# Optimization experiments

Hardware: AMD Instinct MI355X
Metric: run time of the kernel (lower is better)

Reference implementation:

```python
import jax, jax.numpy as jnp
import numpy as np

N = 100000  # number of nodes
SELF_LOOP_W = 2.0  # improved=True in PyG GCNConv


def gcn_conv(x, edge_index, W, b):
    # x: [N, Fin], edge_index: [2, E] (row=src, col=dst), W: [Fin, Fout], b: [Fout]
    src, dst = edge_index[0], edge_index[1]
    h = x @ W  # [N, Fout]
    # degree with improved self-loops (weight 2.0)
    ones = jnp.ones(src.shape, dtype=h.dtype)
    deg = jax.ops.segment_sum(ones, dst, num_segments=N) + SELF_LOOP_W
    dinv = jnp.where(deg > 0, jax.lax.rsqrt(deg), 0.0)
    norm = dinv[src] * dinv[dst]  # [E]
    agg = jax.ops.segment_sum(h[src] * norm[:, None], dst, num_segments=N)
    # self-loop contribution: weight 2.0, norm = dinv_i * 2 * dinv_i
    agg = agg + h * (SELF_LOOP_W * dinv * dinv)[:, None]
    return agg + b


def setup_inputs() -> dict:
    key = jax.random.key(0)
    ks = jax.random.split(key, 6)
    x = jax.random.normal(ks[0], (N, 64), dtype=jnp.float32)
    edge_index = jax.random.randint(ks[1], (2, 1600000), 0, N, dtype=jnp.int64)
    W1 = jax.random.normal(ks[2], (64, 64), dtype=jnp.float32) * 0.1
    b1 = jax.random.normal(ks[3], (64,), dtype=jnp.float32) * 0.1
    W2 = jax.random.normal(ks[4], (64, 32), dtype=jnp.float32) * 0.1
    b2 = jax.random.normal(ks[5], (32,), dtype=jnp.float32) * 0.1
    return {"x": x, "edge_index": edge_index, "W1": W1, "b1": b1, "W2": W2, "b2": b2}


def reference(x, edge_index, W1, b1, W2, b2):
    h1 = jax.nn.relu(gcn_conv(x, edge_index, W1, b1))
    feature_map = h1
    out = gcn_conv(h1, edge_index, W2, b2)
    return (out, feature_map)
```

## Files before the change

kernel.cpp:

```cpp
#include <hip/hip_runtime.h>

#define N_NODES 100000
#define E_EDGES 1600000

#define BSHIFT 7
#define BSIZE 128
#define NBUCK ((N_NODES + BSIZE - 1) / BSIZE)
#define STAGE_TPB 512
#define STAGE_EPT 8
#define STAGE_CHUNK (STAGE_TPB * STAGE_EPT)
#define NREP 2
#define BUCKET_CAP 4096

typedef __attribute__((ext_vector_type(8))) short short8;
typedef __attribute__((ext_vector_type(4))) float float4v;
typedef __attribute__((ext_vector_type(4))) int int4v;
typedef __attribute__((ext_vector_type(4))) unsigned uint4v;

__device__ inline unsigned short f2bf(float f) {
    union { float f; unsigned u; } t; t.f = f;
    unsigned r = (t.u + 0x7fffu + ((t.u >> 16) & 1u)) >> 16;
    return (unsigned short)r;
}
__device__ inline float bf2f(unsigned short h) {
    union { unsigned u; float f; } t; t.u = ((unsigned)h) << 16; return t.f;
}
__device__ inline unsigned pack_bf16x2(float a, float b) {
    return (unsigned)f2bf(a) | ((unsigned)f2bf(b) << 16);
}
__device__ inline float bf_lo(unsigned u) { union { unsigned u; float f; } t; t.u = u << 16; return t.f; }
__device__ inline float bf_hi(unsigned u) { union { unsigned u; float f; } t; t.u = u & 0xffff0000u; return t.f; }

__global__ void cursor_init_kernel(int* __restrict__ gcursor,
                                   unsigned* __restrict__ HS1, unsigned* __restrict__ HS2) {
    int b = blockIdx.x * blockDim.x + threadIdx.x;
    if (b < NBUCK) gcursor[b] = b * BUCKET_CAP;
    if (b < 32) HS1[(size_t)N_NODES * 32 + b] = 0u;
    if (b < 16) HS2[(size_t)N_NODES * 16 + b] = 0u;
}

__global__ void __launch_bounds__(STAGE_TPB) stage_kernel(
    const int* __restrict__ src, const int* __restrict__ dst,
    int* __restrict__ gcursor, unsigned* __restrict__ staged, int E) {
    __shared__ int hist[NREP][NBUCK];
    __shared__ int base[NREP][NBUCK];
    const int tid = threadIdx.x;
    const int rep = (tid >> 8) & (NREP - 1);
    const int e0 = blockIdx.x * STAGE_CHUNK;
    for (int i = tid; i < NREP * NBUCK; i += STAGE_TPB) ((int*)hist)[i] = 0;
    __syncthreads();
    int d[STAGE_EPT], s[STAGE_EPT];
#pragma unroll
    for (int k = 0; k < STAGE_EPT / 4; ++k) {
        int e = e0 + (k * STAGE_TPB + tid) * 4;
        if (e < E) {
            int4v sv = *(const int4v*)(src + e);
            int4v dv = *(const int4v*)(dst + e);
#pragma unroll
            for (int i = 0; i < 4; ++i) {
                s[4 * k + i] = sv[i];
                d[4 * k + i] = dv[i];
                atomicAdd(&hist[rep][dv[i] >> BSHIFT], 1);
            }
        } else {
#pragma unroll
            for (int i = 0; i < 4; ++i) d[4 * k + i] = -1;
        }
    }
    __syncthreads();
    for (int i = tid; i < NBUCK; i += STAGE_TPB) {
        int h0 = hist[0][i], h1 = hist[1][i];
        int t = h0 + h1;
        if (t > 0) {
            int g = atomicAdd(&gcursor[i], t);
            base[0][i] = g;
            base[1][i] = g + h0;
        }
    }
    __syncthreads();
#pragma unroll
    for (int k = 0; k < STAGE_EPT; ++k) {
        if (d[k] >= 0) {
            int b = d[k] >> BSHIFT;
            int pos = atomicAdd(&base[rep][b], 1);
            if (pos < (b + 1) * BUCKET_CAP)
                staged[pos] = (unsigned)s[k] | ((unsigned)(d[k] & (BSIZE - 1)) << 17);
        }
    }
}

__global__ void bscan_kernel(const int* __restrict__ gcursor, int* __restrict__ boff) {
    __shared__ int s[1024];
    const int tid = threadIdx.x;
    int v = 0;
    if (tid < NBUCK) {
        v = gcursor[tid] - tid * BUCKET_CAP;
        if (v > BUCKET_CAP) v = BUCKET_CAP;
        v = (v + 391) & ~3;
    }
    s[tid] = v;
    __syncthreads();
    for (int off = 1; off < 1024; off <<= 1) {
        int t = (tid >= off) ? s[tid - off] : 0;
        __syncthreads();
        s[tid] += t;
        __syncthreads();
    }
    if (tid < NBUCK) boff[tid] = s[tid] - v;
    if (tid == NBUCK - 1) boff[NBUCK] = s[tid];
}

__global__ void bucket_csr_kernel(const unsigned* __restrict__ staged,
                                  const int* __restrict__ gcursor,
                                  const int* __restrict__ boff,
                                  int2* __restrict__ nodeinfo, float* __restrict__ dinv,
                                  int* __restrict__ csrc, int n) {
    __shared__ int ldeg[BSIZE];
    __shared__ int laex[BSIZE];
    __shared__ int lscan[BSIZE];
    __shared__ int lcnt[BSIZE];
    __shared__ unsigned lrec[BUCKET_CAP];
    __shared__ int lsrc[BUCKET_CAP + 512];
    __shared__ int ltot;
    const int b = blockIdx.x;
    const int node0 = b * BSIZE;
    const int nn = min(BSIZE, n - node0);
    const int tid = threadIdx.x;
    if (tid < BSIZE) { ldeg[tid] = 0; lcnt[tid] = 0; }
    __syncthreads();
    const int ebase = boff[b];
    int ecnt = gcursor[b] - b * BUCKET_CAP;
    if (ecnt > BUCKET_CAP) ecnt = BUCKET_CAP;
    const int sbase = b * BUCKET_CAP;
    for (int i = tid; i < ecnt; i += 256) {
        unsigned r = staged[sbase + i];
        lrec[i] = r;
        atomicAdd(&ldeg[r >> 17], 1);
    }
    __syncthreads();
    int mydeg = (tid < BSIZE) ? ldeg[tid] : 0;
    int adeg = (mydeg + 3) & ~3;
    if (tid < BSIZE) lscan[tid] = adeg;
    __syncthreads();
    for (int off = 1; off < BSIZE; off <<= 1) {
        int v = 0;
        if (tid < BSIZE && tid >= off) v = lscan[tid - off];
        __syncthreads();
        if (tid < BSIZE) lscan[tid] += v;
        __syncthreads();
    }
    if (tid < BSIZE) {
        int aex = lscan[tid] - adeg;
        laex[tid] = aex;
        if (tid == BSIZE - 1) ltot = lscan[tid];
        if (tid < nn) {
            nodeinfo[node0 + tid] = make_int2(ebase + aex, mydeg);
            dinv[node0 + tid] = rsqrtf((float)mydeg + 2.0f);
            for (int k = mydeg; k < adeg; ++k) lsrc[aex + k] = N_NODES;
        }
    }
    __syncthreads();
    for (int i = tid; i < ecnt; i += 256) {
        unsigned r = lrec[i];
        int dl = (int)(r >> 17);
        int sv = (int)(r & 0x1FFFFu);
        int pos = laex[dl] + atomicAdd(&lcnt[dl], 1);
        if (pos < BUCKET_CAP + 512) lsrc[pos] = sv;
    }
    __syncthreads();
    const int tot = ltot;
    for (int i = tid; i < tot; i += 256)
        csrc[ebase + i] = lsrc[i];
}

template <int FOUT>
__global__ void __launch_bounds__(256) linear_mfma_kernel(
    const float* __restrict__ X, const float* __restrict__ W,
    const float* __restrict__ dinv, unsigned* __restrict__ HS, int n) {
    constexpr int NT = FOUT / 16;
    constexpr int ROWU = NT * 8;
    const int NTILES_M = n / 16;
    const int lane = threadIdx.x & 63;
    const int gwave = blockIdx.x * 4 + (threadIdx.x >> 6);
    const int nwaves = gridDim.x * 4;
    const int m = lane & 15;
    const int q = lane >> 4;

    short8 Bhi[2][NT], Blo[2][NT];
#pragma unroll
    for (int ks = 0; ks < 2; ++ks)
#pragma unroll
        for (int nt = 0; nt < NT; ++nt) {
            short8 bh, bl;
#pragma unroll
            for (int j = 0; j < 8; ++j) {
                int k = ks * 32 + q * 8 + j;
                float wv = W[k * FOUT + nt * 16 + m];
                unsigned short h = f2bf(wv);
                bh[j] = (short)h;
                bl[j] = (short)f2bf(wv - bf2f(h));
            }
            Bhi[ks][nt] = bh;
            Blo[ks][nt] = bl;
        }

    for (int tile = gwave; tile < NTILES_M; tile += nwaves) {
        const int row0 = tile * 16;
        float4v C[NT];
#pragma unroll
        for (int nt = 0; nt < NT; ++nt) C[nt] = (float4v){0.f, 0.f, 0.f, 0.f};
#pragma unroll
        for (int ks = 0; ks < 2; ++ks) {
            const float* xp = X + (size_t)(row0 + m) * 64 + ks * 32 + q * 8;
            float4v x0 = *(const float4v*)xp;
            float4v x1 = *(const float4v*)(xp + 4);
            short8 Ahi, Alo;
#pragma unroll
            for (int j = 0; j < 4; ++j) {
                unsigned short h0 = f2bf(x0[j]);
                Ahi[j] = (short)h0;
                Alo[j] = (short)f2bf(x0[j] - bf2f(h0));
                unsigned short h1 = f2bf(x1[j]);
                Ahi[4 + j] = (short)h1;
                Alo[4 + j] = (short)f2bf(x1[j] - bf2f(h1));
            }
#pragma unroll
            for (int nt = 0; nt < NT; ++nt) {
                C[nt] = __builtin_amdgcn_mfma_f32_16x16x32_bf16(Ahi, Bhi[ks][nt], C[nt], 0, 0, 0);
                C[nt] = __builtin_amdgcn_mfma_f32_16x16x32_bf16(Alo, Bhi[ks][nt], C[nt], 0, 0, 0);
                C[nt] = __builtin_amdgcn_mfma_f32_16x16x32_bf16(Ahi, Blo[ks][nt], C[nt], 0, 0, 0);
            }
        }
#pragma unroll
        for (int ch = 0; ch < NT / 2; ++ch) {
#pragma unroll
            for (int reg = 0; reg < 4; ++reg) {
                int r = row0 + q * 4 + reg;
                float di = dinv[r];
                unsigned u = pack_bf16x2(C[2 * ch][reg] * di, C[2 * ch + 1][reg] * di);
                HS[(size_t)r * ROWU + ch * 16 + m] = u;
            }
        }
    }
}

template <int ROWU, bool RELU>
__global__ void __launch_bounds__(256) gather_vec_kernel(
    const int2* __restrict__ nodeinfo, const int* __restrict__ csrc,
    const unsigned* __restrict__ HS, const float* __restrict__ dinv,
    const float* __restrict__ bias, float* __restrict__ OUT, int n) {
    constexpr int G = ROWU / 4;
    constexpr int NPB = 256 / G;
    constexpr int FOUT = ROWU * 2;
    const int node = blockIdx.x * NPB + (int)(threadIdx.x / G);
    const int t = threadIdx.x % G;
    if (node >= n) return;
    int2 ni = nodeinfo[node];
    const int start = ni.x;
    const int deg = ni.y;
    const int pend = start + ((deg + 3) & ~3);
    const unsigned* __restrict__ HSt = HS + 4 * t;
    const uint4v own = *(const uint4v*)(HS + (size_t)node * ROWU + 4 * t);
    float alo[4], ahi[4];
#pragma unroll
    for (int k = 0; k < 4; ++k) { alo[k] = 2.0f * bf_lo(own[k]); ahi[k] = 2.0f * bf_hi(own[k]); }
    int j = start;
    for (; j + 8 <= pend; j += 8) {
        int4v s0 = *(const int4v*)(csrc + j);
        int4v s1 = *(const int4v*)(csrc + j + 4);
        uint4v u0 = *(const uint4v*)(HSt + (size_t)s0[0] * ROWU);
        uint4v u1 = *(const uint4v*)(HSt + (size_t)s0[1] * ROWU);
        uint4v u2 = *(const uint4v*)(HSt + (size_t)s0[2] * ROWU);
        uint4v u3 = *(const uint4v*)(HSt + (size_t)s0[3] * ROWU);
        uint4v u4 = *(const uint4v*)(HSt + (size_t)s1[0] * ROWU);
        uint4v u5 = *(const uint4v*)(HSt + (size_t)s1[1] * ROWU);
        uint4v u6 = *(const uint4v*)(HSt + (size_t)s1[2] * ROWU);
        uint4v u7 = *(const uint4v*)(HSt + (size_t)s1[3] * ROWU);
#pragma unroll
        for (int k = 0; k < 4; ++k) {
            float l01 = bf_lo(u0[k]) + bf_lo(u1[k]);
            float l23 = bf_lo(u2[k]) + bf_lo(u3[k]);
            float l45 = bf_lo(u4[k]) + bf_lo(u5[k]);
            float l67 = bf_lo(u6[k]) + bf_lo(u7[k]);
            alo[k] += (l01 + l23) + (l45 + l67);
            float h01 = bf_hi(u0[k]) + bf_hi(u1[k]);
            float h23 = bf_hi(u2[k]) + bf_hi(u3[k]);
            float h45 = bf_hi(u4[k]) + bf_hi(u5[k]);
            float h67 = bf_hi(u6[k]) + bf_hi(u7[k]);
            ahi[k] += (h01 + h23) + (h45 + h67);
        }
    }
    if (j < pend) {
        int4v s0 = *(const int4v*)(csrc + j);
        uint4v u0 = *(const uint4v*)(HSt + (size_t)s0[0] * ROWU);
        uint4v u1 = *(const uint4v*)(HSt + (size_t)s0[1] * ROWU);
        uint4v u2 = *(const uint4v*)(HSt + (size_t)s0[2] * ROWU);
        uint4v u3 = *(const uint4v*)(HSt + (size_t)s0[3] * ROWU);
#pragma unroll
        for (int k = 0; k < 4; ++k) {
            alo[k] += (bf_lo(u0[k]) + bf_lo(u1[k])) + (bf_lo(u2[k]) + bf_lo(u3[k]));
            ahi[k] += (bf_hi(u0[k]) + bf_hi(u1[k])) + (bf_hi(u2[k]) + bf_hi(u3[k]));
        }
    }
    const float dd = dinv[node];
    const int ch = t >> 2;
    const int c0 = (4 * t) & 15;
    const float4v blv = *(const float4v*)(bias + 32 * ch + c0);
    const float4v bhv = *(const float4v*)(bias + 32 * ch + 16 + c0);
    float4v olo, ohi;
#pragma unroll
    for (int k = 0; k < 4; ++k) {
        float o0 = alo[k] * dd + blv[k];
        float o1 = ahi[k] * dd + bhv[k];
        if (RELU) { o0 = fmaxf(o0, 0.0f); o1 = fmaxf(o1, 0.0f); }
        olo[k] = o0;
        ohi[k] = o1;
    }
    float* op = OUT + (size_t)node * FOUT + 32 * ch + c0;
    *(float4v*)op = olo;
    *(float4v*)(op + 16) = ohi;
}

extern "C" void kernel_launch(void* const* d_in, const int* in_sizes, int n_in,
                              void* d_out, int out_size, void* d_ws, size_t ws_size,
                              hipStream_t stream) {
    const float* x  = (const float*)d_in[0];
    const int*   ei = (const int*)d_in[1];
    const float* W1 = (const float*)d_in[2];
    const float* b1 = (const float*)d_in[3];
    const float* W2 = (const float*)d_in[4];
    const float* b2 = (const float*)d_in[5];

    const int* srcp = ei;
    const int* dstp = ei + E_EDGES;

    float* out = (float*)d_out;
    float* fm  = (float*)d_out + N_NODES * 32;

    char* w = (char*)d_ws;
    int*      gcursor  = (int*)w;       w += sizeof(int) * NBUCK;
    int*      boff     = (int*)w;       w += sizeof(int) * (NBUCK + 1);
    int2*     nodeinfo = (int2*)w;      w += sizeof(int2) * N_NODES;
    float*    dinv     = (float*)w;     w += sizeof(float) * N_NODES;
    int*      csrc     = (int*)w;       w += sizeof(int) * (E_EDGES + NBUCK * 392);
    unsigned* staged   = (unsigned*)w;  w += sizeof(unsigned) * (size_t)NBUCK * BUCKET_CAP;
    unsigned* HS1      = (unsigned*)w;  w += sizeof(unsigned) * (size_t)(N_NODES + 1) * 32;
    unsigned* HS2      = (unsigned*)w;  w += sizeof(unsigned) * (size_t)(N_NODES + 1) * 16;

    cursor_init_kernel<<<(NBUCK + 255) / 256, 256, 0, stream>>>(gcursor, HS1, HS2);
    stage_kernel<<<(E_EDGES + STAGE_CHUNK - 1) / STAGE_CHUNK, STAGE_TPB, 0, stream>>>(
        srcp, dstp, gcursor, staged, E_EDGES);
    bscan_kernel<<<1, 1024, 0, stream>>>(gcursor, boff);
    bucket_csr_kernel<<<NBUCK, 256, 0, stream>>>(staged, gcursor, boff, nodeinfo, dinv, csrc, N_NODES);

    linear_mfma_kernel<64><<<512, 256, 0, stream>>>(x, W1, dinv, HS1, N_NODES);
    gather_vec_kernel<32, true><<<(N_NODES + 31) / 32, 256, 0, stream>>>(
        nodeinfo, csrc, HS1, dinv, b1, fm, N_NODES);

    linear_mfma_kernel<32><<<512, 256, 0, stream>>>(fm, W2, dinv, HS2, N_NODES);
    gather_vec_kernel<16, false><<<(N_NODES + 63) / 64, 256, 0, stream>>>(
        nodeinfo, csrc, HS2, dinv, b2, out, N_NODES);
}
```

Measured before the change: 213.0 us.

## Coalesce staged edge writes, degree-sort gather order, add nontemporal hints

The stage kernel now runs a block-local prefix scan over bucket counts and sorts the chunk's records in shared memory. It then writes them to the staged array in contiguous runs instead of scattered per-edge stores. bucket_csr builds a per-bucket node order binned by degree, and the gather kernels process nodes in that order to reduce wave divergence from uneven degrees. Nontemporal loads and stores are added on streaming data, and workspace buffers are aligned to 256 bytes. The costs are extra shared memory, a scan with many barriers in the stage kernel, and an extra indirection through gorder in the gather.

```diff
diff --git a/kernel.cpp b/kernel.cpp
--- a/kernel.cpp
+++ b/kernel.cpp
@@ -43,19 +43,23 @@
     const int* __restrict__ src, const int* __restrict__ dst,
     int* __restrict__ gcursor, unsigned* __restrict__ staged, int E) {
     __shared__ int hist[NREP][NBUCK];
-    __shared__ int base[NREP][NBUCK];
+    __shared__ int dbase[NBUCK];
+    __shared__ int scanw[1024];
+    __shared__ unsigned lrec[STAGE_CHUNK];
+    __shared__ int laddr[STAGE_CHUNK];
     const int tid = threadIdx.x;
     const int rep = (tid >> 8) & (NREP - 1);
     const int e0 = blockIdx.x * STAGE_CHUNK;
     for (int i = tid; i < NREP * NBUCK; i += STAGE_TPB) ((int*)hist)[i] = 0;
+    scanw[tid] = 0; scanw[tid + 512] = 0;
     __syncthreads();
     int d[STAGE_EPT], s[STAGE_EPT];
 #pragma unroll
     for (int k = 0; k < STAGE_EPT / 4; ++k) {
         int e = e0 + (k * STAGE_TPB + tid) * 4;
         if (e < E) {
-            int4v sv = *(const int4v*)(src + e);
-            int4v dv = *(const int4v*)(dst + e);
+            int4v sv = __builtin_nontemporal_load((const int4v*)(src + e));
+            int4v dv = __builtin_nontemporal_load((const int4v*)(dst + e));
 #pragma unroll
             for (int i = 0; i < 4; ++i) {
                 s[4 * k + i] = sv[i];
@@ -68,24 +72,44 @@
         }
     }
     __syncthreads();
+    for (int i = tid; i < NBUCK; i += STAGE_TPB) scanw[i] = hist[0][i] + hist[1][i];
+    if (tid + 512 < NBUCK) scanw[tid + 512] = hist[0][tid + 512] + hist[1][tid + 512];
+    __syncthreads();
+    for (int off = 1; off < 1024; off <<= 1) {
+        int v0 = (tid >= off) ? scanw[tid - off] : 0;
+        int v1 = (tid + 512 >= off) ? scanw[tid + 512 - off] : 0;
+        __syncthreads();
+        scanw[tid] += v0;
+        scanw[tid + 512] += v1;
+        __syncthreads();
+    }
     for (int i = tid; i < NBUCK; i += STAGE_TPB) {
         int h0 = hist[0][i], h1 = hist[1][i];
         int t = h0 + h1;
+        int excl = scanw[i] - t;
         if (t > 0) {
             int g = atomicAdd(&gcursor[i], t);
-            base[0][i] = g;
-            base[1][i] = g + h0;
-        }
+            dbase[i] = g - excl;
+        }
+        hist[0][i] = excl;
+        hist[1][i] = excl + h0;
     }
     __syncthreads();
 #pragma unroll
     for (int k = 0; k < STAGE_EPT; ++k) {
         if (d[k] >= 0) {
             int b = d[k] >> BSHIFT;
-            int pos = atomicAdd(&base[rep][b], 1);
-            if (pos < (b + 1) * BUCKET_CAP)
-                staged[pos] = (unsigned)s[k] | ((unsigned)(d[k] & (BSIZE - 1)) << 17);
-        }
+            int slot = atomicAdd(&hist[rep][b], 1);
+            lrec[slot] = (unsigned)s[k] | ((unsigned)(d[k] & (BSIZE - 1)) << 17);
+            laddr[slot] = dbase[b] + slot;
+        }
+    }
+    __syncthreads();
+    const int total = min(STAGE_CHUNK, E - e0);
+    for (int i = tid; i < total; i += STAGE_TPB) {
+        int a = laddr[i];
+        if ((unsigned)a < (unsigned)(NBUCK * BUCKET_CAP))
+            staged[a] = lrec[i];
     }
 }
 
@@ -114,11 +138,13 @@
                                   const int* __restrict__ gcursor,
                                   const int* __restrict__ boff,
                                   int2* __restrict__ nodeinfo, float* __restrict__ dinv,
-                                  int* __restrict__ csrc, int n) {
+                                  int* __restrict__ csrc, int* __restrict__ gorder, int n) {
     __shared__ int ldeg[BSIZE];
     __shared__ int laex[BSIZE];
     __shared__ int lscan[BSIZE];
     __shared__ int lcnt[BSIZE];
+    __shared__ int h2[32];
+    __shared__ int c2[32];
     __shared__ unsigned lrec[BUCKET_CAP];
     __shared__ int lsrc[BUCKET_CAP + 512];
     __shared__ int ltot;
@@ -127,6 +153,7 @@
     const int nn = min(BSIZE, n - node0);
     const int tid = threadIdx.x;
     if (tid < BSIZE) { ldeg[tid] = 0; lcnt[tid] = 0; }
+    if (tid < 32) { h2[tid] = 0; c2[tid] = 0; }
     __syncthreads();
     const int ebase = boff[b];
     int ecnt = gcursor[b] - b * BUCKET_CAP;
@@ -135,7 +162,7 @@
     for (int i = tid; i < ecnt; i += 256) {
         unsigned r = staged[sbase + i];
         lrec[i] = r;
-        atomicAdd(&ldeg[r >> 17], 1);
+        atomicAdd(&ldeg[(r >> 17) & (BSIZE - 1)], 1);
     }
     __syncthreads();
     int mydeg = (tid < BSIZE) ? ldeg[tid] : 0;
@@ -149,6 +176,7 @@
         if (tid < BSIZE) lscan[tid] += v;
         __syncthreads();
     }
+    const int bin = min(adeg >> 2, 31);
     if (tid < BSIZE) {
         int aex = lscan[tid] - adeg;
         laex[tid] = aex;
@@ -157,12 +185,22 @@
             nodeinfo[node0 + tid] = make_int2(ebase + aex, mydeg);
             dinv[node0 + tid] = rsqrtf((float)mydeg + 2.0f);
             for (int k = mydeg; k < adeg; ++k) lsrc[aex + k] = N_NODES;
-        }
-    }
-    __syncthreads();
+            atomicAdd(&h2[bin], 1);
+        }
+    }
+    __syncthreads();
+    if (tid == 0) {
+        int acc = 0;
+        for (int k = 0; k < 32; ++k) { int v = h2[k]; h2[k] = acc; acc += v; }
+    }
+    __syncthreads();
+    if (tid < nn) {
+        int pos = h2[bin] + atomicAdd(&c2[bin], 1);
+        gorder[node0 + pos] = node0 + tid;
+    }
     for (int i = tid; i < ecnt; i += 256) {
         unsigned r = lrec[i];
-        int dl = (int)(r >> 17);
+        int dl = (int)((r >> 17) & (BSIZE - 1));
         int sv = (int)(r & 0x1FFFFu);
         int pos = laex[dl] + atomicAdd(&lcnt[dl], 1);
         if (pos < BUCKET_CAP + 512) lsrc[pos] = sv;
@@ -212,8 +250,8 @@
 #pragma unroll
         for (int ks = 0; ks < 2; ++ks) {
             const float* xp = X + (size_t)(row0 + m) * 64 + ks * 32 + q * 8;
-            float4v x0 = *(const float4v*)xp;
-            float4v x1 = *(const float4v*)(xp + 4);
+            float4v x0 = __builtin_nontemporal_load((const float4v*)xp);
+            float4v x1 = __builtin_nontemporal_load((const float4v*)(xp + 4));
             short8 Ahi, Alo;
 #pragma unroll
             for (int j = 0; j < 4; ++j) {
@@ -238,7 +276,7 @@
                 int r = row0 + q * 4 + reg;
                 float di = dinv[r];
                 unsigned u = pack_bf16x2(C[2 * ch][reg] * di, C[2 * ch + 1][reg] * di);
-                HS[(size_t)r * ROWU + ch * 16 + m] = u;
+                __builtin_nontemporal_store(u, HS + (size_t)r * ROWU + ch * 16 + m);
             }
         }
     }
@@ -247,14 +285,16 @@
 template <int ROWU, bool RELU>
 __global__ void __launch_bounds__(256) gather_vec_kernel(
     const int2* __restrict__ nodeinfo, const int* __restrict__ csrc,
-    const unsigned* __restrict__ HS, const float* __restrict__ dinv,
-    const float* __restrict__ bias, float* __restrict__ OUT, int n) {
+    const int* __restrict__ gorder, const unsigned* __restrict__ HS,
+    const float* __restrict__ dinv, const float* __restrict__ bias,
+    float* __restrict__ OUT, int n) {
     constexpr int G = ROWU / 4;
     constexpr int NPB = 256 / G;
     constexpr int FOUT = ROWU * 2;
-    const int node = blockIdx.x * NPB + (int)(threadIdx.x / G);
+    const int gslot = blockIdx.x * NPB + (int)(threadIdx.x / G);
     const int t = threadIdx.x % G;
-    if (node >= n) return;
+    if (gslot >= n) return;
+    const int node = gorder[gslot];
     int2 ni = nodeinfo[node];
     const int start = ni.x;
     const int deg = ni.y;
@@ -266,8 +306,8 @@
     for (int k = 0; k < 4; ++k) { alo[k] = 2.0f * bf_lo(own[k]); ahi[k] = 2.0f * bf_hi(own[k]); }
     int j = start;
     for (; j + 8 <= pend; j += 8) {
-        int4v s0 = *(const int4v*)(csrc + j);
-        int4v s1 = *(const int4v*)(csrc + j + 4);
+        int4v s0 = __builtin_nontemporal_load((const int4v*)(csrc + j));
+        int4v s1 = __builtin_nontemporal_load((const int4v*)(csrc + j + 4));
         uint4v u0 = *(const uint4v*)(HSt + (size_t)s0[0] * ROWU);
         uint4v u1 = *(const uint4v*)(HSt + (size_t)s0[1] * ROWU);
         uint4v u2 = *(const uint4v*)(HSt + (size_t)s0[2] * ROWU);
@@ -291,7 +331,7 @@
         }
     }
     if (j < pend) {
-        int4v s0 = *(const int4v*)(csrc + j);
+        int4v s0 = __builtin_nontemporal_load((const int4v*)(csrc + j));
         uint4v u0 = *(const uint4v*)(HSt + (size_t)s0[0] * ROWU);
         uint4v u1 = *(const uint4v*)(HSt + (size_t)s0[1] * ROWU);
         uint4v u2 = *(const uint4v*)(HSt + (size_t)s0[2] * ROWU);
@@ -317,8 +357,8 @@
         ohi[k] = o1;
     }
     float* op = OUT + (size_t)node * FOUT + 32 * ch + c0;
-    *(float4v*)op = olo;
-    *(float4v*)(op + 16) = ohi;
+    __builtin_nontemporal_store(olo, (float4v*)op);
+    __builtin_nontemporal_store(ohi, (float4v*)(op + 16));
 }
 
 extern "C" void kernel_launch(void* const* d_in, const int* in_sizes, int n_in,
@@ -338,26 +378,33 @@
     float* fm  = (float*)d_out + N_NODES * 32;
 
     char* w = (char*)d_ws;
-    int*      gcursor  = (int*)w;       w += sizeof(int) * NBUCK;
-    int*      boff     = (int*)w;       w += sizeof(int) * (NBUCK + 1);
-    int2*     nodeinfo = (int2*)w;      w += sizeof(int2) * N_NODES;
-    float*    dinv     = (float*)w;     w += sizeof(float) * N_NODES;
-    int*      csrc     = (int*)w;       w += sizeof(int) * (E_EDGES + NBUCK * 392);
-    unsigned* staged   = (unsigned*)w;  w += sizeof(unsigned) * (size_t)NBUCK * BUCKET_CAP;
-    unsigned* HS1      = (unsigned*)w;  w += sizeof(unsigned) * (size_t)(N_NODES + 1) * 32;
-    unsigned* HS2      = (unsigned*)w;  w += sizeof(unsigned) * (size_t)(N_NODES + 1) * 16;
+    auto alloc = [&w](size_t bytes) -> void* {
+        uintptr_t p = ((uintptr_t)w + 255) & ~(uintptr_t)255;
+        w = (char*)(p + bytes);
+        return (void*)p;
+    };
+    int*      gcursor  = (int*)alloc(sizeof(int) * NBUCK);
+    int*      boff     = (int*)alloc(sizeof(int) * (NBUCK + 1));
+    int2*     nodeinfo = (int2*)alloc(sizeof(int2) * N_NODES);
+    float*    dinv     = (float*)alloc(sizeof(float) * N_NODES);
+    int*      gorder   = (int*)alloc(sizeof(int) * N_NODES);
+    int*      csrc     = (int*)alloc(sizeof(int) * (E_EDGES + NBUCK * 392));
+    unsigned* staged   = (unsigned*)alloc(sizeof(unsigned) * (size_t)NBUCK * BUCKET_CAP);
+    unsigned* HS1      = (unsigned*)alloc(sizeof(unsigned) * (size_t)(N_NODES + 1) * 32);
+    unsigned* HS2      = (unsigned*)alloc(sizeof(unsigned) * (size_t)(N_NODES + 1) * 16);
 
     cursor_init_kernel<<<(NBUCK + 255) / 256, 256, 0, stream>>>(gcursor, HS1, HS2);
     stage_kernel<<<(E_EDGES + STAGE_CHUNK - 1) / STAGE_CHUNK, STAGE_TPB, 0, stream>>>(
         srcp, dstp, gcursor, staged, E_EDGES);
     bscan_kernel<<<1, 1024, 0, stream>>>(gcursor, boff);
-    bucket_csr_kernel<<<NBUCK, 256, 0, stream>>>(staged, gcursor, boff, nodeinfo, dinv, csrc, N_NODES);
+    bucket_csr_kernel<<<NBUCK, 256, 0, stream>>>(staged, gcursor, boff, nodeinfo, dinv,
+                                                 csrc, gorder, N_NODES);
 
     linear_mfma_kernel<64><<<512, 256, 0, stream>>>(x, W1, dinv, HS1, N_NODES);
     gather_vec_kernel<32, true><<<(N_NODES + 31) / 32, 256, 0, stream>>>(
-        nodeinfo, csrc, HS1, dinv, b1, fm, N_NODES);
+        nodeinfo, csrc, gorder, HS1, dinv, b1, fm, N_NODES);
 
     linear_mfma_kernel<32><<<512, 256, 0, stream>>>(fm, W2, dinv, HS2, N_NODES);
     gather_vec_kernel<16, false><<<(N_NODES + 63) / 64, 256, 0, stream>>>(
-        nodeinfo, csrc, HS2, dinv, b2, out, N_NODES);
-}
+        nodeinfo, csrc, gorder, HS2, dinv, b2, out, N_NODES);
+}
```

Result: faster. 204.3 us (-4.1%).
